# Optimization experiments

Measured on AMD Instinct MI355X. Metric: run time of the kernel, lower is better.

## Reference

```python
import jax, jax.numpy as jnp
import numpy as np

N = 50000
E = 600000
D = 128
BN_EPS = 1e-5
GIN_EPS = 0.0  # init_eps=0, not learned


def setup_inputs() -> dict:
    key = jax.random.key(0)
    ks = jax.random.split(key, 8)
    x = jax.random.normal(ks[0], (N, D), dtype=jnp.float32)
    edge_index = jax.random.randint(ks[1], (2, E), 0, N, dtype=jnp.int64)
    s = 1.0 / np.sqrt(D)
    w1 = jax.random.uniform(ks[2], (D, D), jnp.float32, -s, s)
    b1 = jax.random.uniform(ks[3], (D,), jnp.float32, -s, s)
    w2 = jax.random.uniform(ks[4], (D, D), jnp.float32, -s, s)
    b2 = jax.random.uniform(ks[5], (D,), jnp.float32, -s, s)
    gamma = jnp.ones((D,), jnp.float32)
    beta = jnp.zeros((D,), jnp.float32)
    return {"x": x, "edge_index": edge_index, "w1": w1, "b1": b1,
            "w2": w2, "b2": b2, "gamma": gamma, "beta": beta}


def reference(x, edge_index, w1, b1, w2, b2, gamma, beta):
    src, dst = edge_index[0], edge_index[1]
    # GINConv sum aggregation: out[i] = sum_{(j,i) in E} x[j]
    agg = jax.ops.segment_sum(x[src], dst, num_segments=N)  # [N, D]
    h = (1.0 + GIN_EPS) * x + agg
    # 2-layer MLP (Linear-ReLU-Linear)
    h = jax.nn.relu(h @ w1 + b1)
    h = h @ w2 + b2
    # training-mode BatchNorm over nodes (biased variance)
    mean = jnp.mean(h, axis=0)
    var = jnp.var(h, axis=0)
    h = (h - mean) * jax.lax.rsqrt(var + BN_EPS) * gamma + beta
    h = jax.nn.relu(h)
    # residual (in_dim == out_dim); dropout p=0.0 -> identity
    return x + h
```

## Files before the change

kernel.cpp:

```cpp
#include <hip/hip_runtime.h>
#include <hip/hip_cooperative_groups.h>

namespace cg = cooperative_groups;

#define NN 50000
#define EE 600000
#define DD 128
#define MAXDEG 64
#define NSLICE 32
#define EPT 8

typedef __attribute__((ext_vector_type(8))) short short8;
typedef __attribute__((ext_vector_type(4))) float f32x4;

static __device__ __forceinline__ unsigned short f2bf(float f) {
    unsigned int u = __float_as_uint(f);
    u += 0x7FFF + ((u >> 16) & 1);
    return (unsigned short)(u >> 16);
}
static __device__ __forceinline__ float bflo(unsigned int u) {
    return __uint_as_float(u << 16);
}
static __device__ __forceinline__ float bfhi(unsigned int u) {
    return __uint_as_float(u & 0xFFFF0000u);
}


static __device__ __forceinline__ void gemm32(const unsigned short* __restrict__ A,
                                              const unsigned short* __restrict__ W,
                                              const float* __restrict__ bias,
                                              unsigned short* __restrict__ C,
                                              float* __restrict__ priv,
                                              int lane, int row0, int relu, int unit) {
    int m = lane & 15, quad = lane >> 4;
    short8 af[2][4];
    #pragma unroll
    for (int mt = 0; mt < 2; ++mt) {
        int gr = row0 + mt * 16 + m;
        #pragma unroll
        for (int kc = 0; kc < 4; ++kc)
            af[mt][kc] = (gr < NN) ? *(const short8*)&A[gr * 128 + kc * 32 + quad * 8]
                                   : (short8)0;
    }
    f32x4 acc[2][8];
    #pragma unroll
    for (int mt = 0; mt < 2; ++mt)
        #pragma unroll
        for (int i = 0; i < 8; ++i) acc[mt][i] = (f32x4)0.f;

    #pragma unroll
    for (int h = 0; h < 2; ++h) {
        short8 wf[4][4];
        #pragma unroll
        for (int nt = 0; nt < 4; ++nt)
            #pragma unroll
            for (int kc = 0; kc < 4; ++kc)
                wf[nt][kc] = *(const short8*)&W[(h * 64 + nt * 16 + m) * 128 + kc * 32 + quad * 8];
        #pragma unroll
        for (int kc = 0; kc < 4; ++kc)
            #pragma unroll
            for (int nt = 0; nt < 4; ++nt) {
                acc[0][h * 4 + nt] = __builtin_amdgcn_mfma_f32_16x16x32_bf16(af[0][kc], wf[nt][kc], acc[0][h * 4 + nt], 0, 0, 0);
                acc[1][h * 4 + nt] = __builtin_amdgcn_mfma_f32_16x16x32_bf16(af[1][kc], wf[nt][kc], acc[1][h * 4 + nt], 0, 0, 0);
            }
    }

    if (relu) {
        #pragma unroll
        for (int nt = 0; nt < 8; ++nt) {
            int col = nt * 16 + m;
            float bv = bias[col];
            #pragma unroll
            for (int mt = 0; mt < 2; ++mt)
                #pragma unroll
                for (int r = 0; r < 4; ++r) {
                    int gr = row0 + mt * 16 + quad * 4 + r;
                    if (gr < NN) C[gr * 128 + col] = f2bf(fmaxf(acc[mt][nt][r] + bv, 0.f));
                }
        }
    } else {
        float* myslice = priv + (unit & (NSLICE - 1)) * 2 * DD;
        #pragma unroll
        for (int nt = 0; nt < 8; ++nt) {
            int col = nt * 16 + m;
            float bv = bias[col];
            float s = 0.f, sq = 0.f;
            #pragma unroll
            for (int mt = 0; mt < 2; ++mt)
                #pragma unroll
                for (int r = 0; r < 4; ++r) {
                    int gr = row0 + mt * 16 + quad * 4 + r;
                    if (gr < NN) {
                        float v = acc[mt][nt][r] + bv;
                        C[gr * 128 + col] = f2bf(v);
                        s += v;
                        sq += v * v;
                    }
                }
            s  += __shfl_down(s, 32, 64);  sq += __shfl_down(sq, 32, 64);
            s  += __shfl_down(s, 16, 64);  sq += __shfl_down(sq, 16, 64);
            if (quad == 0) {
                atomicAdd(&myslice[col], s);
                atomicAdd(&myslice[DD + col], sq);
            }
        }
    }
}

static __device__ __forceinline__ void agg_node(int node, int lane,
                                                const unsigned int* __restrict__ xb,
                                                const int* __restrict__ cursor,
                                                const unsigned short* __restrict__ srcPad,
                                                unsigned int* __restrict__ h0) {
    int cnt = cursor[node];
    if (cnt > MAXDEG) cnt = MAXDEG;
    int sv = srcPad[(node << 6) + lane];
    unsigned int self = xb[(node << 6) + lane];
    float ax = bflo(self), ay = bfhi(self);
    int j = 0;
    for (; j + 8 <= cnt; j += 8) {
        int a0 = __shfl(sv, j, 64),     a1 = __shfl(sv, j + 1, 64);
        int a2 = __shfl(sv, j + 2, 64), a3 = __shfl(sv, j + 3, 64);
        int a4 = __shfl(sv, j + 4, 64), a5 = __shfl(sv, j + 5, 64);
        int a6 = __shfl(sv, j + 6, 64), a7 = __shfl(sv, j + 7, 64);
        unsigned int u0 = xb[(a0 << 6) + lane], u1 = xb[(a1 << 6) + lane];
        unsigned int u2 = xb[(a2 << 6) + lane], u3 = xb[(a3 << 6) + lane];
        unsigned int u4 = xb[(a4 << 6) + lane], u5 = xb[(a5 << 6) + lane];
        unsigned int u6 = xb[(a6 << 6) + lane], u7 = xb[(a7 << 6) + lane];
        ax += bflo(u0) + bflo(u1) + bflo(u2) + bflo(u3)
            + bflo(u4) + bflo(u5) + bflo(u6) + bflo(u7);
        ay += bfhi(u0) + bfhi(u1) + bfhi(u2) + bfhi(u3)
            + bfhi(u4) + bfhi(u5) + bfhi(u6) + bfhi(u7);
    }
    for (; j + 4 <= cnt; j += 4) {
        int a0 = __shfl(sv, j, 64),     a1 = __shfl(sv, j + 1, 64);
        int a2 = __shfl(sv, j + 2, 64), a3 = __shfl(sv, j + 3, 64);
        unsigned int u0 = xb[(a0 << 6) + lane], u1 = xb[(a1 << 6) + lane];
        unsigned int u2 = xb[(a2 << 6) + lane], u3 = xb[(a3 << 6) + lane];
        ax += bflo(u0) + bflo(u1) + bflo(u2) + bflo(u3);
        ay += bfhi(u0) + bfhi(u1) + bfhi(u2) + bfhi(u3);
    }
    for (; j < cnt; ++j) {
        int s = __shfl(sv, j, 64);
        unsigned int u = xb[(s << 6) + lane];
        ax += bflo(u);
        ay += bfhi(u);
    }
    h0[(node << 6) + lane] = (unsigned int)f2bf(ax) | ((unsigned int)f2bf(ay) << 16);
}


__global__ __launch_bounds__(256) void k_all(const float* __restrict__ x,
                                             const int* __restrict__ ei,
                                             const float* __restrict__ w1,
                                             const float* __restrict__ b1,
                                             const float* __restrict__ w2,
                                             const float* __restrict__ b2,
                                             const float* __restrict__ gamma,
                                             const float* __restrict__ beta,
                                             float* __restrict__ out,
                                             char* __restrict__ wsb) {
    cg::grid_group grid = cg::this_grid();
    int*            cursor = (int*)wsb;
    float*          priv   = (float*)(wsb + 0x31000);
    unsigned short* srcPad = (unsigned short*)(wsb + 0x40000);
    unsigned int*   xb     = (unsigned int*)(wsb + 0x680000);
    unsigned int*   h0w    = (unsigned int*)(wsb + 0x1300000);
    unsigned short* h1b    = (unsigned short*)(wsb + 0x1F80000);
    unsigned int*   h2w    = (unsigned int*)(wsb + 0x2C00000);
    unsigned short* wt     = (unsigned short*)(wsb + 0x3880000);
    const unsigned short* h0b = (const unsigned short*)h0w;
    unsigned short*       h2b = (unsigned short*)h2w;

    int nth = gridDim.x * 256;
    int nwave = nth >> 6;
    int tid = blockIdx.x * 256 + threadIdx.x;
    int lane = tid & 63;
    int gwave = tid >> 6;

    for (int i = tid; i < NN; i += nth) cursor[i] = 0;
    for (int i = tid; i < NSLICE * 2 * DD; i += nth) priv[i] = 0.f;
    grid.sync();

    for (int e = tid; e < EE; e += nth) {
        int s = ei[e];
        int d = ei[EE + e];
        int pos = atomicAdd(&cursor[d], 1);
        if (pos < MAXDEG) srcPad[(d << 6) + pos] = (unsigned short)s;
    }
    for (int i = tid; i < 32768; i += nth) {
        int w = i >> 14, idx = i & 16383;
        int k = idx >> 7, n = idx & 127;
        const float* src = w ? w2 : w1;
        wt[w * 16384 + n * 128 + k] = f2bf(src[k * 128 + n]);
    }
    for (int xi = tid; xi < NN * DD / 2; xi += nth) {
        float2 v = ((const float2*)x)[xi];
        xb[xi] = (unsigned int)f2bf(v.x) | ((unsigned int)f2bf(v.y) << 16);
    }
    grid.sync();

    for (int node = gwave; node < NN; node += nwave)
        agg_node(node, lane, xb, cursor, srcPad, h0w);
    grid.sync();

    for (int unit = gwave; unit * 32 < NN; unit += nwave)
        gemm32(h0b, wt, b1, h1b, nullptr, lane, unit * 32, 1, unit);
    grid.sync();

    for (int unit = gwave; unit * 32 < NN; unit += nwave)
        gemm32(h1b, wt + 16384, b2, h2b, priv, lane, unit * 32, 0, unit);
    grid.sync();

    __shared__ float ssc[DD], ssh[DD];
    int t = threadIdx.x;
    if (t < DD) {
        float s = 0.f, sq = 0.f;
        #pragma unroll
        for (int sl = 0; sl < NSLICE; ++sl) {
            s  += priv[sl * 2 * DD + t];
            sq += priv[sl * 2 * DD + DD + t];
        }
        float mean = s * (1.0f / NN);
        float var = fmaxf(sq * (1.0f / NN) - mean * mean, 0.f);
        float sc = gamma[t] * rsqrtf(var + 1e-5f);
        ssc[t] = sc;
        ssh[t] = beta[t] - mean * sc;
    }
    __syncthreads();
    for (int idx = tid; idx < NN * DD / 4; idx += nth) {
        int c0 = (idx & 31) * 4;
        unsigned int p0 = h2w[2 * idx];
        unsigned int p1 = h2w[2 * idx + 1];
        float4 xv = ((const float4*)x)[idx];
        float4 o;
        o.x = xv.x + fmaxf(fmaf(bflo(p0), ssc[c0 + 0], ssh[c0 + 0]), 0.f);
        o.y = xv.y + fmaxf(fmaf(bfhi(p0), ssc[c0 + 1], ssh[c0 + 1]), 0.f);
        o.z = xv.z + fmaxf(fmaf(bflo(p1), ssc[c0 + 2], ssh[c0 + 2]), 0.f);
        o.w = xv.w + fmaxf(fmaf(bfhi(p1), ssc[c0 + 3], ssh[c0 + 3]), 0.f);
        ((float4*)out)[idx] = o;
    }
}


__global__ __launch_bounds__(256) void k_prep(const float* __restrict__ w1,
                                              const float* __restrict__ w2,
                                              const float* __restrict__ x,
                                              const int* __restrict__ ei,
                                              int* __restrict__ cursor,
                                              unsigned short* __restrict__ srcPad,
                                              unsigned short* __restrict__ wt,
                                              unsigned int* __restrict__ xb) {
    int tid = blockIdx.x * 256 + threadIdx.x;
    if (tid < EE / EPT) {
        #pragma unroll
        for (int i = 0; i < EPT; ++i) {
            int e = tid + i * (EE / EPT);
            int s = ei[e];
            int d = ei[EE + e];
            int pos = atomicAdd(&cursor[d], 1);
            if (pos < MAXDEG) srcPad[(d << 6) + pos] = (unsigned short)s;
        }
    }
    if (tid < 32768) {
        int w = tid >> 14, idx = tid & 16383;
        int k = idx >> 7, n = idx & 127;
        const float* src = w ? w2 : w1;
        wt[w * 16384 + n * 128 + k] = f2bf(src[k * 128 + n]);
    }
    int xi = tid - 32768;
    if (xi >= 0 && xi < NN * DD / 2) {
        float2 v = ((const float2*)x)[xi];
        xb[xi] = (unsigned int)f2bf(v.x) | ((unsigned int)f2bf(v.y) << 16);
    }
}

__global__ __launch_bounds__(256) void k_agg(const unsigned int* __restrict__ xb,
                                             const int* __restrict__ cursor,
                                             const unsigned short* __restrict__ srcPad,
                                             unsigned int* __restrict__ h0) {
    int wave = (blockIdx.x * blockDim.x + threadIdx.x) >> 6;
    int lane = threadIdx.x & 63;
    if (wave >= NN) return;
    agg_node(wave, lane, xb, cursor, srcPad, h0);
}

__global__ __launch_bounds__(256) void k_gemm(const unsigned short* __restrict__ A,
                                              const unsigned short* __restrict__ W,
                                              const float* __restrict__ bias,
                                              unsigned short* __restrict__ Cb,
                                              float* __restrict__ priv,
                                              int relu) {
    int wave = (blockIdx.x * 256 + threadIdx.x) >> 6;
    int lane = threadIdx.x & 63;
    int row0 = wave * 32;
    if (row0 >= NN) return;
    gemm32(A, W, bias, Cb, priv, lane, row0, relu, wave);
}

__global__ __launch_bounds__(256) void k_final(const float* __restrict__ x,
                                               const unsigned int* __restrict__ h2,
                                               float* __restrict__ out,
                                               const float* __restrict__ priv,
                                               const float* __restrict__ gamma,
                                               const float* __restrict__ beta) {
    __shared__ float ssc[DD], ssh[DD];
    int t = threadIdx.x;
    if (t < DD) {
        float s = 0.f, sq = 0.f;
        #pragma unroll
        for (int sl = 0; sl < NSLICE; ++sl) {
            s  += priv[sl * 2 * DD + t];
            sq += priv[sl * 2 * DD + DD + t];
        }
        float mean = s * (1.0f / NN);
        float var = fmaxf(sq * (1.0f / NN) - mean * mean, 0.f);
        float sc = gamma[t] * rsqrtf(var + 1e-5f);
        ssc[t] = sc;
        ssh[t] = beta[t] - mean * sc;
    }
    __syncthreads();
    #pragma unroll
    for (int u = 0; u < 4; ++u) {
        int idx = blockIdx.x * 1024 + u * 256 + t;
        if (idx >= NN * DD / 4) return;
        int c0 = (idx & 31) * 4;
        unsigned int p0 = h2[2 * idx];
        unsigned int p1 = h2[2 * idx + 1];
        float4 xv = ((const float4*)x)[idx];
        float4 o;
        o.x = xv.x + fmaxf(fmaf(bflo(p0), ssc[c0 + 0], ssh[c0 + 0]), 0.f);
        o.y = xv.y + fmaxf(fmaf(bfhi(p0), ssc[c0 + 1], ssh[c0 + 1]), 0.f);
        o.z = xv.z + fmaxf(fmaf(bflo(p1), ssc[c0 + 2], ssh[c0 + 2]), 0.f);
        o.w = xv.w + fmaxf(fmaf(bfhi(p1), ssc[c0 + 3], ssh[c0 + 3]), 0.f);
        ((float4*)out)[idx] = o;
    }
}

extern "C" void kernel_launch(void* const* d_in, const int* in_sizes, int n_in,
                              void* d_out, int out_size, void* d_ws, size_t ws_size,
                              hipStream_t stream) {
    (void)in_sizes; (void)n_in; (void)out_size; (void)ws_size;
    const float* x     = (const float*)d_in[0];
    const int*   ei    = (const int*)d_in[1];
    const float* w1    = (const float*)d_in[2];
    const float* b1    = (const float*)d_in[3];
    const float* w2    = (const float*)d_in[4];
    const float* b2    = (const float*)d_in[5];
    const float* gamma = (const float*)d_in[6];
    const float* beta  = (const float*)d_in[7];
    float* out = (float*)d_out;
    char* wsb  = (char*)d_ws;

    int*            cursor = (int*)wsb;
    float*          priv   = (float*)(wsb + 0x31000);
    unsigned short* srcPad = (unsigned short*)(wsb + 0x40000);
    unsigned int*   xb     = (unsigned int*)(wsb + 0x680000);
    unsigned int*   h0w    = (unsigned int*)(wsb + 0x1300000);
    unsigned short* h1b    = (unsigned short*)(wsb + 0x1F80000);
    unsigned int*   h2w    = (unsigned int*)(wsb + 0x2C00000);
    unsigned short* wt     = (unsigned short*)(wsb + 0x3880000);
    const unsigned short* h0b = (const unsigned short*)h0w;
    unsigned short*       h2b = (unsigned short*)h2w;

    bool coop_ok = false;
    int dev = 0;
    if (hipGetDevice(&dev) == hipSuccess) {
        int has_coop = 0;
        if (hipDeviceGetAttribute(&has_coop, hipDeviceAttributeCooperativeLaunch, dev) == hipSuccess
            && has_coop) {
            int blocks_per_cu = 0;
            if (hipOccupancyMaxActiveBlocksPerMultiprocessor(
                    &blocks_per_cu, reinterpret_cast<const void*>(&k_all), 256, 0) == hipSuccess
                && blocks_per_cu > 0) {
                int nb = blocks_per_cu * 256;
                if (nb > 2048) nb = 2048;
                void* args[] = {(void*)&x, (void*)&ei, (void*)&w1, (void*)&b1, (void*)&w2,
                                (void*)&b2, (void*)&gamma, (void*)&beta, (void*)&out, (void*)&wsb};
                if (hipLaunchCooperativeKernel(reinterpret_cast<const void*>(&k_all),
                                               dim3(nb), dim3(256), args, 0, stream) == hipSuccess)
                    coop_ok = true;
            }
        }
    }
    if (coop_ok) return;

    (void)hipMemsetAsync(wsb, 0, 0x39000, stream);
    k_prep<<<(32768 + NN * DD / 2 + 255) / 256, 256, 0, stream>>>(w1, w2, x, ei, cursor, srcPad, wt, xb);
    k_agg<<<(NN * 64 + 255) / 256, 256, 0, stream>>>(xb, cursor, srcPad, h0w);
    k_gemm<<<(NN + 127) / 128, 256, 0, stream>>>(h0b, wt, b1, h1b, nullptr, 1);
    k_gemm<<<(NN + 127) / 128, 256, 0, stream>>>(h1b, wt + 16384, b2, h2b, priv, 0);
    k_final<<<(NN * DD / 4 + 1023) / 1024, 256, 0, stream>>>(x, h2w, out, priv, gamma, beta);
}
```

Baseline: 182.4 us.

## Fuse aggregation with both MLP GEMMs per 16-node tile in LDS

The cooperative kernel now has each wave aggregate 16 nodes straight into a shared-memory tile, then run both MLP layers on that tile with MFMA, writing only the second-layer output and BN partial sums. The h0/h1 global intermediates and two grid-wide syncs go away, and the workspace zeroing moves to a host memset ahead of the launch, removing another grid sync. The x-to-bf16 conversion is widened to float4. In exchange, weights are reloaded from global memory for every 16-row unit with less reuse than the 32-row GEMM, the extra LDS may lower occupancy, and the gather's latency is no longer separated from the GEMM work.

Result: slower. 325.0 us (+78.2%).

```diff
diff --git a/kernel.cpp b/kernel.cpp
--- a/kernel.cpp
+++ b/kernel.cpp
@@ -9,6 +9,8 @@
 #define MAXDEG 64
 #define NSLICE 32
 #define EPT 8
+#define RST 136
+#define UNITS (NN / 16)
 
 typedef __attribute__((ext_vector_type(8))) short short8;
 typedef __attribute__((ext_vector_type(4))) float f32x4;
@@ -23,6 +25,69 @@
 }
 static __device__ __forceinline__ float bfhi(unsigned int u) {
     return __uint_as_float(u & 0xFFFF0000u);
+}
+
+static __device__ __forceinline__ void gemm16(unsigned short* tile,
+                                              const unsigned short* __restrict__ W,
+                                              const float* __restrict__ bias,
+                                              unsigned short* __restrict__ h2b,
+                                              float* __restrict__ priv,
+                                              int lane, int base, int relu, int unit) {
+    int m = lane & 15, quad = lane >> 4;
+    short8 af[4];
+    #pragma unroll
+    for (int kc = 0; kc < 4; ++kc)
+        af[kc] = *(const short8*)&tile[m * RST + kc * 32 + quad * 8];
+    f32x4 acc[8];
+    #pragma unroll
+    for (int i = 0; i < 8; ++i) acc[i] = (f32x4)0.f;
+
+    #pragma unroll
+    for (int h = 0; h < 2; ++h) {
+        short8 wf[4][4];
+        #pragma unroll
+        for (int nt = 0; nt < 4; ++nt)
+            #pragma unroll
+            for (int kc = 0; kc < 4; ++kc)
+                wf[nt][kc] = *(const short8*)&W[(h * 64 + nt * 16 + m) * 128 + kc * 32 + quad * 8];
+        #pragma unroll
+        for (int kc = 0; kc < 4; ++kc)
+            #pragma unroll
+            for (int nt = 0; nt < 4; ++nt)
+                acc[h * 4 + nt] = __builtin_amdgcn_mfma_f32_16x16x32_bf16(af[kc], wf[nt][kc], acc[h * 4 + nt], 0, 0, 0);
+    }
+
+    if (relu) {
+        #pragma unroll
+        for (int nt = 0; nt < 8; ++nt) {
+            int col = nt * 16 + m;
+            float bv = bias[col];
+            #pragma unroll
+            for (int r = 0; r < 4; ++r)
+                tile[(quad * 4 + r) * RST + col] = f2bf(fmaxf(acc[nt][r] + bv, 0.f));
+        }
+    } else {
+        float* myslice = priv + (unit & (NSLICE - 1)) * 2 * DD;
+        #pragma unroll
+        for (int nt = 0; nt < 8; ++nt) {
+            int col = nt * 16 + m;
+            float bv = bias[col];
+            float s = 0.f, sq = 0.f;
+            #pragma unroll
+            for (int r = 0; r < 4; ++r) {
+                float v = acc[nt][r] + bv;
+                h2b[(base + quad * 4 + r) * 128 + col] = f2bf(v);
+                s += v;
+                sq += v * v;
+            }
+            s  += __shfl_down(s, 32, 64);  sq += __shfl_down(sq, 32, 64);
+            s  += __shfl_down(s, 16, 64);  sq += __shfl_down(sq, 16, 64);
+            if (quad == 0) {
+                atomicAdd(&myslice[col], s);
+                atomicAdd(&myslice[DD + col], sq);
+            }
+        }
+    }
 }
 
 
@@ -165,12 +230,12 @@
     float*          priv   = (float*)(wsb + 0x31000);
     unsigned short* srcPad = (unsigned short*)(wsb + 0x40000);
     unsigned int*   xb     = (unsigned int*)(wsb + 0x680000);
-    unsigned int*   h0w    = (unsigned int*)(wsb + 0x1300000);
-    unsigned short* h1b    = (unsigned short*)(wsb + 0x1F80000);
     unsigned int*   h2w    = (unsigned int*)(wsb + 0x2C00000);
     unsigned short* wt     = (unsigned short*)(wsb + 0x3880000);
-    const unsigned short* h0b = (const unsigned short*)h0w;
-    unsigned short*       h2b = (unsigned short*)h2w;
+    unsigned short* h2b    = (unsigned short*)h2w;
+
+    __shared__ __align__(16) unsigned short tiles[4][16 * RST];
+    __shared__ float ssc[DD], ssh[DD];
 
     int nth = gridDim.x * 256;
     int nwave = nth >> 6;
@@ -178,10 +243,6 @@
     int lane = tid & 63;
     int gwave = tid >> 6;
 
-    for (int i = tid; i < NN; i += nth) cursor[i] = 0;
-    for (int i = tid; i < NSLICE * 2 * DD; i += nth) priv[i] = 0.f;
-    grid.sync();
-
     for (int e = tid; e < EE; e += nth) {
         int s = ei[e];
         int d = ei[EE + e];
@@ -194,25 +255,74 @@
         const float* src = w ? w2 : w1;
         wt[w * 16384 + n * 128 + k] = f2bf(src[k * 128 + n]);
     }
-    for (int xi = tid; xi < NN * DD / 2; xi += nth) {
-        float2 v = ((const float2*)x)[xi];
-        xb[xi] = (unsigned int)f2bf(v.x) | ((unsigned int)f2bf(v.y) << 16);
+    for (int xi = tid; xi < NN * DD / 4; xi += nth) {
+        float4 v = ((const float4*)x)[xi];
+        uint2 p;
+        p.x = (unsigned int)f2bf(v.x) | ((unsigned int)f2bf(v.y) << 16);
+        p.y = (unsigned int)f2bf(v.z) | ((unsigned int)f2bf(v.w) << 16);
+        ((uint2*)xb)[xi] = p;
     }
     grid.sync();
 
-    for (int node = gwave; node < NN; node += nwave)
-        agg_node(node, lane, xb, cursor, srcPad, h0w);
+    {
+        unsigned short* tile = tiles[threadIdx.x >> 6];
+        for (int unit = gwave; unit < UNITS; unit += nwave) {
+            int base = unit * 16;
+            #pragma unroll
+            for (int half = 0; half < 2; ++half) {
+                int ct8[8], sv8[8];
+                unsigned int self8[8];
+                #pragma unroll
+                for (int i = 0; i < 8; ++i) {
+                    int node = base + half * 8 + i;
+                    ct8[i]   = cursor[node];
+                    sv8[i]   = srcPad[(node << 6) + lane];
+                    self8[i] = xb[(node << 6) + lane];
+                }
+                #pragma unroll
+                for (int i = 0; i < 8; ++i) {
+                    int cnt = ct8[i] > MAXDEG ? MAXDEG : ct8[i];
+                    int sv = sv8[i];
+                    float ax = bflo(self8[i]), ay = bfhi(self8[i]);
+                    int j = 0;
+                    for (; j + 8 <= cnt; j += 8) {
+                        int a0 = __shfl(sv, j, 64),     a1 = __shfl(sv, j + 1, 64);
+                        int a2 = __shfl(sv, j + 2, 64), a3 = __shfl(sv, j + 3, 64);
+                        int a4 = __shfl(sv, j + 4, 64), a5 = __shfl(sv, j + 5, 64);
+                        int a6 = __shfl(sv, j + 6, 64), a7 = __shfl(sv, j + 7, 64);
+                        unsigned int u0 = xb[(a0 << 6) + lane], u1 = xb[(a1 << 6) + lane];
+                        unsigned int u2 = xb[(a2 << 6) + lane], u3 = xb[(a3 << 6) + lane];
+                        unsigned int u4 = xb[(a4 << 6) + lane], u5 = xb[(a5 << 6) + lane];
+                        unsigned int u6 = xb[(a6 << 6) + lane], u7 = xb[(a7 << 6) + lane];
+                        ax += bflo(u0) + bflo(u1) + bflo(u2) + bflo(u3)
+                            + bflo(u4) + bflo(u5) + bflo(u6) + bflo(u7);
+                        ay += bfhi(u0) + bfhi(u1) + bfhi(u2) + bfhi(u3)
+                            + bfhi(u4) + bfhi(u5) + bfhi(u6) + bfhi(u7);
+                    }
+                    for (; j + 4 <= cnt; j += 4) {
+                        int a0 = __shfl(sv, j, 64),     a1 = __shfl(sv, j + 1, 64);
+                        int a2 = __shfl(sv, j + 2, 64), a3 = __shfl(sv, j + 3, 64);
+                        unsigned int u0 = xb[(a0 << 6) + lane], u1 = xb[(a1 << 6) + lane];
+                        unsigned int u2 = xb[(a2 << 6) + lane], u3 = xb[(a3 << 6) + lane];
+                        ax += bflo(u0) + bflo(u1) + bflo(u2) + bflo(u3);
+                        ay += bfhi(u0) + bfhi(u1) + bfhi(u2) + bfhi(u3);
+                    }
+                    for (; j < cnt; ++j) {
+                        int s = __shfl(sv, j, 64);
+                        unsigned int u = xb[(s << 6) + lane];
+                        ax += bflo(u);
+                        ay += bfhi(u);
+                    }
+                    ((unsigned int*)(tile + (half * 8 + i) * RST))[lane] =
+                        (unsigned int)f2bf(ax) | ((unsigned int)f2bf(ay) << 16);
+                }
+            }
+            gemm16(tile, wt,         b1, nullptr, nullptr, lane, base, 1, unit);
+            gemm16(tile, wt + 16384, b2, h2b,     priv,    lane, base, 0, unit);
+        }
+    }
     grid.sync();
 
-    for (int unit = gwave; unit * 32 < NN; unit += nwave)
-        gemm32(h0b, wt, b1, h1b, nullptr, lane, unit * 32, 1, unit);
-    grid.sync();
-
-    for (int unit = gwave; unit * 32 < NN; unit += nwave)
-        gemm32(h1b, wt + 16384, b2, h2b, priv, lane, unit * 32, 0, unit);
-    grid.sync();
-
-    __shared__ float ssc[DD], ssh[DD];
     int t = threadIdx.x;
     if (t < DD) {
         float s = 0.f, sq = 0.f;
@@ -362,6 +472,8 @@
     unsigned short* wt     = (unsigned short*)(wsb + 0x3880000);
     const unsigned short* h0b = (const unsigned short*)h0w;
     unsigned short*       h2b = (unsigned short*)h2w;
+
+    (void)hipMemsetAsync(wsb, 0, 0x39000, stream);
 
     bool coop_ok = false;
     int dev = 0;
@@ -385,7 +497,6 @@
     }
     if (coop_ok) return;
 
-    (void)hipMemsetAsync(wsb, 0, 0x39000, stream);
     k_prep<<<(32768 + NN * DD / 2 + 255) / 256, 256, 0, stream>>>(w1, w2, x, ei, cursor, srcPad, wt, xb);
     k_agg<<<(NN * 64 + 255) / 256, 256, 0, stream>>>(xb, cursor, srcPad, h0w);
     k_gemm<<<(NN + 127) / 128, 256, 0, stream>>>(h0b, wt, b1, h1b, nullptr, 1);
```

## Fuse aggregation and both MLP GEMMs per 16-row tile in LDS

Applied to the files above, without the earlier changes.

Replaces the cooperative persistent kernel with grid syncs, and the separate agg/gemm launches, with one fused kernel. Each wave aggregates 16 nodes into an LDS tile and runs both MFMA GEMMs on that tile, so h0 and h1 never go to global memory. Neighbor metadata for 8 nodes is prefetched at a time, and x is converted to bf16 with float4 loads. The cost is lower MFMA reuse, since each wave handles 16 rows instead of 32 and reloads the weights per wave. It also adds LDS use and relies on NN being divisible by 16.

After: 188.8 us. +3.5%, slower.

```diff
diff --git a/kernel.cpp b/kernel.cpp
--- a/kernel.cpp
+++ b/kernel.cpp
@@ -1,7 +1,4 @@
 #include <hip/hip_runtime.h>
-#include <hip/hip_cooperative_groups.h>
-
-namespace cg = cooperative_groups;
 
 #define NN 50000
 #define EE 600000
@@ -9,6 +6,8 @@
 #define MAXDEG 64
 #define NSLICE 32
 #define EPT 8
+#define RST 136
+#define UNITS (NN / 16)
 
 typedef __attribute__((ext_vector_type(8))) short short8;
 typedef __attribute__((ext_vector_type(4))) float f32x4;
@@ -25,28 +24,20 @@
     return __uint_as_float(u & 0xFFFF0000u);
 }
 
-
-static __device__ __forceinline__ void gemm32(const unsigned short* __restrict__ A,
+static __device__ __forceinline__ void gemm16(unsigned short* tile,
                                               const unsigned short* __restrict__ W,
                                               const float* __restrict__ bias,
-                                              unsigned short* __restrict__ C,
+                                              unsigned short* __restrict__ h2b,
                                               float* __restrict__ priv,
-                                              int lane, int row0, int relu, int unit) {
+                                              int lane, int base, int relu, int unit) {
     int m = lane & 15, quad = lane >> 4;
-    short8 af[2][4];
-    #pragma unroll
-    for (int mt = 0; mt < 2; ++mt) {
-        int gr = row0 + mt * 16 + m;
-        #pragma unroll
-        for (int kc = 0; kc < 4; ++kc)
-            af[mt][kc] = (gr < NN) ? *(const short8*)&A[gr * 128 + kc * 32 + quad * 8]
-                                   : (short8)0;
-    }
-    f32x4 acc[2][8];
-    #pragma unroll
-    for (int mt = 0; mt < 2; ++mt)
-        #pragma unroll
-        for (int i = 0; i < 8; ++i) acc[mt][i] = (f32x4)0.f;
+    short8 af[4];
+    #pragma unroll
+    for (int kc = 0; kc < 4; ++kc)
+        af[kc] = *(const short8*)&tile[m * RST + kc * 32 + quad * 8];
+    f32x4 acc[8];
+    #pragma unroll
+    for (int i = 0; i < 8; ++i) acc[i] = (f32x4)0.f;
 
     #pragma unroll
     for (int h = 0; h < 2; ++h) {
@@ -59,10 +50,8 @@
         #pragma unroll
         for (int kc = 0; kc < 4; ++kc)
             #pragma unroll
-            for (int nt = 0; nt < 4; ++nt) {
-                acc[0][h * 4 + nt] = __builtin_amdgcn_mfma_f32_16x16x32_bf16(af[0][kc], wf[nt][kc], acc[0][h * 4 + nt], 0, 0, 0);
-                acc[1][h * 4 + nt] = __builtin_amdgcn_mfma_f32_16x16x32_bf16(af[1][kc], wf[nt][kc], acc[1][h * 4 + nt], 0, 0, 0);
-            }
+            for (int nt = 0; nt < 4; ++nt)
+                acc[h * 4 + nt] = __builtin_amdgcn_mfma_f32_16x16x32_bf16(af[kc], wf[nt][kc], acc[h * 4 + nt], 0, 0, 0);
     }
 
     if (relu) {
@@ -71,12 +60,8 @@
             int col = nt * 16 + m;
             float bv = bias[col];
             #pragma unroll
-            for (int mt = 0; mt < 2; ++mt)
-                #pragma unroll
-                for (int r = 0; r < 4; ++r) {
-                    int gr = row0 + mt * 16 + quad * 4 + r;
-                    if (gr < NN) C[gr * 128 + col] = f2bf(fmaxf(acc[mt][nt][r] + bv, 0.f));
-                }
+            for (int r = 0; r < 4; ++r)
+                tile[(quad * 4 + r) * RST + col] = f2bf(fmaxf(acc[nt][r] + bv, 0.f));
         }
     } else {
         float* myslice = priv + (unit & (NSLICE - 1)) * 2 * DD;
@@ -86,17 +71,12 @@
             float bv = bias[col];
             float s = 0.f, sq = 0.f;
             #pragma unroll
-            for (int mt = 0; mt < 2; ++mt)
-                #pragma unroll
-                for (int r = 0; r < 4; ++r) {
-                    int gr = row0 + mt * 16 + quad * 4 + r;
-                    if (gr < NN) {
-                        float v = acc[mt][nt][r] + bv;
-                        C[gr * 128 + col] = f2bf(v);
-                        s += v;
-                        sq += v * v;
-                    }
-                }
+            for (int r = 0; r < 4; ++r) {
+                float v = acc[nt][r] + bv;
+                h2b[(base + quad * 4 + r) * 128 + col] = f2bf(v);
+                s += v;
+                sq += v * v;
+            }
             s  += __shfl_down(s, 32, 64);  sq += __shfl_down(sq, 32, 64);
             s  += __shfl_down(s, 16, 64);  sq += __shfl_down(sq, 16, 64);
             if (quad == 0) {
@@ -104,141 +84,6 @@
                 atomicAdd(&myslice[DD + col], sq);
             }
         }
-    }
-}
-
-static __device__ __forceinline__ void agg_node(int node, int lane,
-                                                const unsigned int* __restrict__ xb,
-                                                const int* __restrict__ cursor,
-                                                const unsigned short* __restrict__ srcPad,
-                                                unsigned int* __restrict__ h0) {
-    int cnt = cursor[node];
-    if (cnt > MAXDEG) cnt = MAXDEG;
-    int sv = srcPad[(node << 6) + lane];
-    unsigned int self = xb[(node << 6) + lane];
-    float ax = bflo(self), ay = bfhi(self);
-    int j = 0;
-    for (; j + 8 <= cnt; j += 8) {
-        int a0 = __shfl(sv, j, 64),     a1 = __shfl(sv, j + 1, 64);
-        int a2 = __shfl(sv, j + 2, 64), a3 = __shfl(sv, j + 3, 64);
-        int a4 = __shfl(sv, j + 4, 64), a5 = __shfl(sv, j + 5, 64);
-        int a6 = __shfl(sv, j + 6, 64), a7 = __shfl(sv, j + 7, 64);
-        unsigned int u0 = xb[(a0 << 6) + lane], u1 = xb[(a1 << 6) + lane];
-        unsigned int u2 = xb[(a2 << 6) + lane], u3 = xb[(a3 << 6) + lane];
-        unsigned int u4 = xb[(a4 << 6) + lane], u5 = xb[(a5 << 6) + lane];
-        unsigned int u6 = xb[(a6 << 6) + lane], u7 = xb[(a7 << 6) + lane];
-        ax += bflo(u0) + bflo(u1) + bflo(u2) + bflo(u3)
-            + bflo(u4) + bflo(u5) + bflo(u6) + bflo(u7);
-        ay += bfhi(u0) + bfhi(u1) + bfhi(u2) + bfhi(u3)
-            + bfhi(u4) + bfhi(u5) + bfhi(u6) + bfhi(u7);
-    }
-    for (; j + 4 <= cnt; j += 4) {
-        int a0 = __shfl(sv, j, 64),     a1 = __shfl(sv, j + 1, 64);
-        int a2 = __shfl(sv, j + 2, 64), a3 = __shfl(sv, j + 3, 64);
-        unsigned int u0 = xb[(a0 << 6) + lane], u1 = xb[(a1 << 6) + lane];
-        unsigned int u2 = xb[(a2 << 6) + lane], u3 = xb[(a3 << 6) + lane];
-        ax += bflo(u0) + bflo(u1) + bflo(u2) + bflo(u3);
-        ay += bfhi(u0) + bfhi(u1) + bfhi(u2) + bfhi(u3);
-    }
-    for (; j < cnt; ++j) {
-        int s = __shfl(sv, j, 64);
-        unsigned int u = xb[(s << 6) + lane];
-        ax += bflo(u);
-        ay += bfhi(u);
-    }
-    h0[(node << 6) + lane] = (unsigned int)f2bf(ax) | ((unsigned int)f2bf(ay) << 16);
-}
-
-
-__global__ __launch_bounds__(256) void k_all(const float* __restrict__ x,
-                                             const int* __restrict__ ei,
-                                             const float* __restrict__ w1,
-                                             const float* __restrict__ b1,
-                                             const float* __restrict__ w2,
-                                             const float* __restrict__ b2,
-                                             const float* __restrict__ gamma,
-                                             const float* __restrict__ beta,
-                                             float* __restrict__ out,
-                                             char* __restrict__ wsb) {
-    cg::grid_group grid = cg::this_grid();
-    int*            cursor = (int*)wsb;
-    float*          priv   = (float*)(wsb + 0x31000);
-    unsigned short* srcPad = (unsigned short*)(wsb + 0x40000);
-    unsigned int*   xb     = (unsigned int*)(wsb + 0x680000);
-    unsigned int*   h0w    = (unsigned int*)(wsb + 0x1300000);
-    unsigned short* h1b    = (unsigned short*)(wsb + 0x1F80000);
-    unsigned int*   h2w    = (unsigned int*)(wsb + 0x2C00000);
-    unsigned short* wt     = (unsigned short*)(wsb + 0x3880000);
-    const unsigned short* h0b = (const unsigned short*)h0w;
-    unsigned short*       h2b = (unsigned short*)h2w;
-
-    int nth = gridDim.x * 256;
-    int nwave = nth >> 6;
-    int tid = blockIdx.x * 256 + threadIdx.x;
-    int lane = tid & 63;
-    int gwave = tid >> 6;
-
-    for (int i = tid; i < NN; i += nth) cursor[i] = 0;
-    for (int i = tid; i < NSLICE * 2 * DD; i += nth) priv[i] = 0.f;
-    grid.sync();
-
-    for (int e = tid; e < EE; e += nth) {
-        int s = ei[e];
-        int d = ei[EE + e];
-        int pos = atomicAdd(&cursor[d], 1);
-        if (pos < MAXDEG) srcPad[(d << 6) + pos] = (unsigned short)s;
-    }
-    for (int i = tid; i < 32768; i += nth) {
-        int w = i >> 14, idx = i & 16383;
-        int k = idx >> 7, n = idx & 127;
-        const float* src = w ? w2 : w1;
-        wt[w * 16384 + n * 128 + k] = f2bf(src[k * 128 + n]);
-    }
-    for (int xi = tid; xi < NN * DD / 2; xi += nth) {
-        float2 v = ((const float2*)x)[xi];
-        xb[xi] = (unsigned int)f2bf(v.x) | ((unsigned int)f2bf(v.y) << 16);
-    }
-    grid.sync();
-
-    for (int node = gwave; node < NN; node += nwave)
-        agg_node(node, lane, xb, cursor, srcPad, h0w);
-    grid.sync();
-
-    for (int unit = gwave; unit * 32 < NN; unit += nwave)
-        gemm32(h0b, wt, b1, h1b, nullptr, lane, unit * 32, 1, unit);
-    grid.sync();
-
-    for (int unit = gwave; unit * 32 < NN; unit += nwave)
-        gemm32(h1b, wt + 16384, b2, h2b, priv, lane, unit * 32, 0, unit);
-    grid.sync();
-
-    __shared__ float ssc[DD], ssh[DD];
-    int t = threadIdx.x;
-    if (t < DD) {
-        float s = 0.f, sq = 0.f;
-        #pragma unroll
-        for (int sl = 0; sl < NSLICE; ++sl) {
-            s  += priv[sl * 2 * DD + t];
-            sq += priv[sl * 2 * DD + DD + t];
-        }
-        float mean = s * (1.0f / NN);
-        float var = fmaxf(sq * (1.0f / NN) - mean * mean, 0.f);
-        float sc = gamma[t] * rsqrtf(var + 1e-5f);
-        ssc[t] = sc;
-        ssh[t] = beta[t] - mean * sc;
-    }
-    __syncthreads();
-    for (int idx = tid; idx < NN * DD / 4; idx += nth) {
-        int c0 = (idx & 31) * 4;
-        unsigned int p0 = h2w[2 * idx];
-        unsigned int p1 = h2w[2 * idx + 1];
-        float4 xv = ((const float4*)x)[idx];
-        float4 o;
-        o.x = xv.x + fmaxf(fmaf(bflo(p0), ssc[c0 + 0], ssh[c0 + 0]), 0.f);
-        o.y = xv.y + fmaxf(fmaf(bfhi(p0), ssc[c0 + 1], ssh[c0 + 1]), 0.f);
-        o.z = xv.z + fmaxf(fmaf(bflo(p1), ssc[c0 + 2], ssh[c0 + 2]), 0.f);
-        o.w = xv.w + fmaxf(fmaf(bfhi(p1), ssc[c0 + 3], ssh[c0 + 3]), 0.f);
-        ((float4*)out)[idx] = o;
     }
 }
 
@@ -269,34 +114,85 @@
         wt[w * 16384 + n * 128 + k] = f2bf(src[k * 128 + n]);
     }
     int xi = tid - 32768;
-    if (xi >= 0 && xi < NN * DD / 2) {
-        float2 v = ((const float2*)x)[xi];
-        xb[xi] = (unsigned int)f2bf(v.x) | ((unsigned int)f2bf(v.y) << 16);
-    }
-}
-
-__global__ __launch_bounds__(256) void k_agg(const unsigned int* __restrict__ xb,
-                                             const int* __restrict__ cursor,
-                                             const unsigned short* __restrict__ srcPad,
-                                             unsigned int* __restrict__ h0) {
-    int wave = (blockIdx.x * blockDim.x + threadIdx.x) >> 6;
+    if (xi >= 0 && xi < NN * DD / 4) {
+        float4 v = ((const float4*)x)[xi];
+        uint2 p;
+        p.x = (unsigned int)f2bf(v.x) | ((unsigned int)f2bf(v.y) << 16);
+        p.y = (unsigned int)f2bf(v.z) | ((unsigned int)f2bf(v.w) << 16);
+        ((uint2*)xb)[xi] = p;
+    }
+}
+
+
+__global__ __launch_bounds__(256) void k_fused(const unsigned int* __restrict__ xb,
+                                               const int* __restrict__ cursor,
+                                               const unsigned short* __restrict__ srcPad,
+                                               const unsigned short* __restrict__ wt,
+                                               const float* __restrict__ b1,
+                                               const float* __restrict__ b2,
+                                               unsigned short* __restrict__ h2b,
+                                               float* __restrict__ priv) {
+    __shared__ __align__(16) unsigned short tiles[4][16 * RST];
+    int wid  = threadIdx.x >> 6;
     int lane = threadIdx.x & 63;
-    if (wave >= NN) return;
-    agg_node(wave, lane, xb, cursor, srcPad, h0);
-}
-
-__global__ __launch_bounds__(256) void k_gemm(const unsigned short* __restrict__ A,
-                                              const unsigned short* __restrict__ W,
-                                              const float* __restrict__ bias,
-                                              unsigned short* __restrict__ Cb,
-                                              float* __restrict__ priv,
-                                              int relu) {
-    int wave = (blockIdx.x * 256 + threadIdx.x) >> 6;
-    int lane = threadIdx.x & 63;
-    int row0 = wave * 32;
-    if (row0 >= NN) return;
-    gemm32(A, W, bias, Cb, priv, lane, row0, relu, wave);
-}
+    int unit = blockIdx.x * 4 + wid;
+    if (unit >= UNITS) return;
+    unsigned short* tile = tiles[wid];
+    int base = unit * 16;
+
+    #pragma unroll
+    for (int half = 0; half < 2; ++half) {
+        int ct8[8], sv8[8];
+        unsigned int self8[8];
+        #pragma unroll
+        for (int i = 0; i < 8; ++i) {
+            int node = base + half * 8 + i;
+            ct8[i]   = cursor[node];
+            sv8[i]   = srcPad[(node << 6) + lane];
+            self8[i] = xb[(node << 6) + lane];
+        }
+        #pragma unroll
+        for (int i = 0; i < 8; ++i) {
+            int cnt = ct8[i] > MAXDEG ? MAXDEG : ct8[i];
+            int sv = sv8[i];
+            float ax = bflo(self8[i]), ay = bfhi(self8[i]);
+            int j = 0;
+            for (; j + 8 <= cnt; j += 8) {
+                int a0 = __shfl(sv, j, 64),     a1 = __shfl(sv, j + 1, 64);
+                int a2 = __shfl(sv, j + 2, 64), a3 = __shfl(sv, j + 3, 64);
+                int a4 = __shfl(sv, j + 4, 64), a5 = __shfl(sv, j + 5, 64);
+                int a6 = __shfl(sv, j + 6, 64), a7 = __shfl(sv, j + 7, 64);
+                unsigned int u0 = xb[(a0 << 6) + lane], u1 = xb[(a1 << 6) + lane];
+                unsigned int u2 = xb[(a2 << 6) + lane], u3 = xb[(a3 << 6) + lane];
+                unsigned int u4 = xb[(a4 << 6) + lane], u5 = xb[(a5 << 6) + lane];
+                unsigned int u6 = xb[(a6 << 6) + lane], u7 = xb[(a7 << 6) + lane];
+                ax += bflo(u0) + bflo(u1) + bflo(u2) + bflo(u3)
+                    + bflo(u4) + bflo(u5) + bflo(u6) + bflo(u7);
+                ay += bfhi(u0) + bfhi(u1) + bfhi(u2) + bfhi(u3)
+                    + bfhi(u4) + bfhi(u5) + bfhi(u6) + bfhi(u7);
+            }
+            for (; j + 4 <= cnt; j += 4) {
+                int a0 = __shfl(sv, j, 64),     a1 = __shfl(sv, j + 1, 64);
+                int a2 = __shfl(sv, j + 2, 64), a3 = __shfl(sv, j + 3, 64);
+                unsigned int u0 = xb[(a0 << 6) + lane], u1 = xb[(a1 << 6) + lane];
+                unsigned int u2 = xb[(a2 << 6) + lane], u3 = xb[(a3 << 6) + lane];
+                ax += bflo(u0) + bflo(u1) + bflo(u2) + bflo(u3);
+                ay += bfhi(u0) + bfhi(u1) + bfhi(u2) + bfhi(u3);
+            }
+            for (; j < cnt; ++j) {
+                int s = __shfl(sv, j, 64);
+                unsigned int u = xb[(s << 6) + lane];
+                ax += bflo(u);
+                ay += bfhi(u);
+            }
+            ((unsigned int*)(tile + (half * 8 + i) * RST))[lane] =
+                (unsigned int)f2bf(ax) | ((unsigned int)f2bf(ay) << 16);
+        }
+    }
+    gemm16(tile, wt,         b1, nullptr, nullptr, lane, base, 1, unit);
+    gemm16(tile, wt + 16384, b2, h2b,     priv,    lane, base, 0, unit);
+}
+
 
 __global__ __launch_bounds__(256) void k_final(const float* __restrict__ x,
                                                const unsigned int* __restrict__ h2,
@@ -356,39 +252,13 @@
     float*          priv   = (float*)(wsb + 0x31000);
     unsigned short* srcPad = (unsigned short*)(wsb + 0x40000);
     unsigned int*   xb     = (unsigned int*)(wsb + 0x680000);
-    unsigned int*   h0w    = (unsigned int*)(wsb + 0x1300000);
-    unsigned short* h1b    = (unsigned short*)(wsb + 0x1F80000);
     unsigned int*   h2w    = (unsigned int*)(wsb + 0x2C00000);
     unsigned short* wt     = (unsigned short*)(wsb + 0x3880000);
-    const unsigned short* h0b = (const unsigned short*)h0w;
-    unsigned short*       h2b = (unsigned short*)h2w;
-
-    bool coop_ok = false;
-    int dev = 0;
-    if (hipGetDevice(&dev) == hipSuccess) {
-        int has_coop = 0;
-        if (hipDeviceGetAttribute(&has_coop, hipDeviceAttributeCooperativeLaunch, dev) == hipSuccess
-            && has_coop) {
-            int blocks_per_cu = 0;
-            if (hipOccupancyMaxActiveBlocksPerMultiprocessor(
-                    &blocks_per_cu, reinterpret_cast<const void*>(&k_all), 256, 0) == hipSuccess
-                && blocks_per_cu > 0) {
-                int nb = blocks_per_cu * 256;
-                if (nb > 2048) nb = 2048;
-                void* args[] = {(void*)&x, (void*)&ei, (void*)&w1, (void*)&b1, (void*)&w2,
-                                (void*)&b2, (void*)&gamma, (void*)&beta, (void*)&out, (void*)&wsb};
-                if (hipLaunchCooperativeKernel(reinterpret_cast<const void*>(&k_all),
-                                               dim3(nb), dim3(256), args, 0, stream) == hipSuccess)
-                    coop_ok = true;
-            }
-        }
-    }
-    if (coop_ok) return;
+    unsigned short* h2b    = (unsigned short*)h2w;
 
     (void)hipMemsetAsync(wsb, 0, 0x39000, stream);
-    k_prep<<<(32768 + NN * DD / 2 + 255) / 256, 256, 0, stream>>>(w1, w2, x, ei, cursor, srcPad, wt, xb);
-    k_agg<<<(NN * 64 + 255) / 256, 256, 0, stream>>>(xb, cursor, srcPad, h0w);
-    k_gemm<<<(NN + 127) / 128, 256, 0, stream>>>(h0b, wt, b1, h1b, nullptr, 1);
-    k_gemm<<<(NN + 127) / 128, 256, 0, stream>>>(h1b, wt + 16384, b2, h2b, priv, 0);
+
+    k_prep <<<(32768 + NN * DD / 4 + 255) / 256, 256, 0, stream>>>(w1, w2, x, ei, cursor, srcPad, wt, xb);
+    k_fused<<<(UNITS + 3) / 4, 256, 0, stream>>>(xb, cursor, srcPad, wt, b1, b2, h2b, priv);
     k_final<<<(NN * DD / 4 + 1023) / 1024, 256, 0, stream>>>(x, h2w, out, priv, gamma, beta);
 }
```
